# Kernel optimization log

Measured on AMD Instinct MI355X. Metric: run time of the kernel, lower is better.

## Reference

```python
import jax, jax.numpy as jnp
import numpy as np

N_EMBD = 1024
N_HEAD = 16
HEAD_SIZE = N_EMBD // N_HEAD
EPS = 1e-5


def layernorm(x, g, b):
    mu = jnp.mean(x, axis=-1, keepdims=True)
    var = jnp.var(x, axis=-1, keepdims=True)
    return (x - mu) * jax.lax.rsqrt(var + EPS) * g + b


def setup_inputs() -> dict:
    key = jax.random.key(0)
    ks = jax.random.split(key, 12)
    s = 0.02
    C = N_EMBD
    return {
        "x": jax.random.normal(ks[0], (2, 2048, C), dtype=jnp.float32),
        "Wq": jax.random.normal(ks[1], (C, C), dtype=jnp.float32) * s,
        "Wk": jax.random.normal(ks[2], (C, C), dtype=jnp.float32) * s,
        "Wv": jax.random.normal(ks[3], (C, C), dtype=jnp.float32) * s,
        "Wo": jax.random.normal(ks[4], (C, C), dtype=jnp.float32) * s,
        "bo": jnp.zeros((C,), dtype=jnp.float32),
        "W1": jax.random.normal(ks[5], (C, 4 * C), dtype=jnp.float32) * s,
        "b1": jnp.zeros((4 * C,), dtype=jnp.float32),
        "W2": jax.random.normal(ks[6], (4 * C, C), dtype=jnp.float32) * s,
        "b2": jnp.zeros((C,), dtype=jnp.float32),
        "ln1_g": jnp.ones((C,), dtype=jnp.float32),
        "ln1_b": jnp.zeros((C,), dtype=jnp.float32),
        "ln2_g": jnp.ones((C,), dtype=jnp.float32),
        "ln2_b": jnp.zeros((C,), dtype=jnp.float32),
    }


def reference(x, Wq, Wk, Wv, Wo, bo, W1, b1, W2, b2, ln1_g, ln1_b, ln2_g, ln2_b):
    B, T, C = x.shape
    H, Dh = N_HEAD, HEAD_SIZE

    # --- self-attention branch ---
    h = layernorm(x, ln1_g, ln1_b)
    q = (h @ Wq).reshape(B, T, H, Dh)
    k = (h @ Wk).reshape(B, T, H, Dh)
    v = (h @ Wv).reshape(B, T, H, Dh)

    # NOTE: original scales by C**-0.5 (n_embd), not head_size**-0.5
    scale = C ** (-0.5)
    scores = jnp.einsum("bqhd,bkhd->bhqk", q, k) * scale  # [B,H,T,T]
    causal = jnp.tril(jnp.ones((T, T), dtype=bool))
    scores = jnp.where(causal, scores, -jnp.inf)
    wei = jax.nn.softmax(scores, axis=-1)
    attn = jnp.einsum("bhqk,bkhd->bqhd", wei, v).reshape(B, T, C)
    x = x + attn @ Wo + bo

    # --- MLP branch ---
    h2 = layernorm(x, ln2_g, ln2_b)
    ff = jax.nn.relu(h2 @ W1 + b1) @ W2 + b2
    return x + ff
```

## Files before the change

kernel.cpp:

```cpp
#include <hip/hip_runtime.h>

typedef unsigned short u16;
typedef __bf16 bf16;
typedef bf16 bf16x8 __attribute__((ext_vector_type(8)));
typedef float f32x4 __attribute__((ext_vector_type(4)));


__device__ __forceinline__ u16 f2bf(float f) {
  bf16 b = (bf16)f;
  return __builtin_bit_cast(u16, b);
}

__device__ __forceinline__ void gll16(void* lds, const void* g) {
  __builtin_amdgcn_global_load_lds((__attribute__((address_space(1))) void*)g,
                                   (__attribute__((address_space(3))) void*)lds,
                                   16, 0, 0);
}

__device__ __forceinline__ f32x4 mfma16(bf16x8 a, bf16x8 b, f32x4 c) {
  return __builtin_amdgcn_mfma_f32_16x16x32_bf16(a, b, c, 0, 0, 0);
}


__global__ __launch_bounds__(256)
void transpose_all(const float* __restrict__ Wq, const float* __restrict__ Wk,
                   const float* __restrict__ Wv, const float* __restrict__ Wo,
                   const float* __restrict__ W1, const float* __restrict__ W2,
                   u16* __restrict__ WqT, u16* __restrict__ WkT,
                   u16* __restrict__ WvT, u16* __restrict__ WoT,
                   u16* __restrict__ W1T, u16* __restrict__ W2T) {
  __shared__ float tile[32][33];
  const int id = blockIdx.x;
  const float* src;
  u16* dst;
  int R, C, t;
  if (id < 4096) {
    const int w = id >> 10;
    t = id & 1023; R = 1024; C = 1024;
    src = w == 0 ? Wq : w == 1 ? Wk : w == 2 ? Wv : Wo;
    dst = w == 0 ? WqT : w == 1 ? WkT : w == 2 ? WvT : WoT;
  } else if (id < 8192) {
    t = id - 4096; R = 1024; C = 4096; src = W1; dst = W1T;
  } else {
    t = id - 8192; R = 4096; C = 1024; src = W2; dst = W2T;
  }
  const int tilesx = C >> 5;
  const int c0 = (t % tilesx) * 32, r0 = (t / tilesx) * 32;
  const int tx = threadIdx.x, ty = threadIdx.y;
#pragma unroll
  for (int i = 0; i < 4; ++i)
    tile[ty + i * 8][tx] = src[(size_t)(r0 + ty + i * 8) * C + c0 + tx];
  __syncthreads();
#pragma unroll
  for (int i = 0; i < 4; ++i)
    dst[(size_t)(c0 + ty + i * 8) * R + r0 + tx] = f2bf(tile[tx][ty + i * 8]);
}


__global__ __launch_bounds__(256)
void ln_kernel(const float* __restrict__ x, const float* __restrict__ g,
               const float* __restrict__ bb, u16* __restrict__ h) {
  const int row = blockIdx.x;
  const int tid = threadIdx.x;
  const float4 xv = ((const float4*)(x + (size_t)row * 1024))[tid];
  float s = xv.x + xv.y + xv.z + xv.w;
  float q = xv.x * xv.x + xv.y * xv.y + xv.z * xv.z + xv.w * xv.w;
#pragma unroll
  for (int m = 1; m < 64; m <<= 1) {
    s += __shfl_xor(s, m);
    q += __shfl_xor(q, m);
  }
  __shared__ float ss[4], qq[4];
  const int wid = tid >> 6, lane = tid & 63;
  if (lane == 0) { ss[wid] = s; qq[wid] = q; }
  __syncthreads();
  s = ss[0] + ss[1] + ss[2] + ss[3];
  q = qq[0] + qq[1] + qq[2] + qq[3];
  const float mean = s * (1.0f / 1024.0f);
  const float var = q * (1.0f / 1024.0f) - mean * mean;
  const float rs = rsqrtf(var + 1e-5f);
  const float4 gv = ((const float4*)g)[tid];
  const float4 bv = ((const float4*)bb)[tid];
  ushort4 o;
  o.x = f2bf((xv.x - mean) * rs * gv.x + bv.x);
  o.y = f2bf((xv.y - mean) * rs * gv.y + bv.y);
  o.z = f2bf((xv.z - mean) * rs * gv.z + bv.z);
  o.w = f2bf((xv.w - mean) * rs * gv.w + bv.w);
  ((ushort4*)(h + (size_t)row * 1024))[tid] = o;
}


__device__ __forceinline__ void xcd_swizzle(int& bx, int& by, int& bz) {
  const int gx = gridDim.x, gy = gridDim.y;
  const int nwg = gx * gy * (int)gridDim.z;
  int flat = (int)blockIdx.x + gx * ((int)blockIdx.y + gy * (int)blockIdx.z);
  flat = (flat & 7) * (nwg >> 3) + (flat >> 3);
  bx = flat % gx;
  const int rem = flat / gx;
  by = rem % gy;
  bz = rem / gy;
}


template <int EPI>
__global__ __launch_bounds__(256)
void gemm_bt(const u16* __restrict__ A, const u16* __restrict__ Bt,
             const float* __restrict__ bias,
             void* __restrict__ O0, void* __restrict__ O1, void* __restrict__ O2,
             int M, int N, int K) {
  __shared__ __align__(16) u16 Alds[3][128 * 32];
  __shared__ __align__(16) u16 Blds[3][128 * 32];
  const int tid = threadIdx.x;
  const int lane = tid & 63, wid = tid >> 6;
  const int rl = lane & 15, kg = lane >> 4;
  const int ksw = (rl >> 1) & 3;
  int bx, by, bz;
  xcd_swizzle(bx, by, bz);
  const int m0 = by * 128, n0 = bx * 128;
  f32x4 acc[4][4];
#pragma unroll
  for (int i = 0; i < 4; ++i)
#pragma unroll
    for (int j = 0; j < 4; ++j) acc[i][j] = (f32x4){0.f, 0.f, 0.f, 0.f};
  const int wr = wid >> 1, wc = wid & 1;
  const int c0 = wid * 2, c1 = wid * 2 + 1;
  const int srow0 = c0 * 16 + (lane >> 2);
  const int srow1 = c1 * 16 + (lane >> 2);
  const int skol = (((lane & 3) ^ ((lane >> 3) & 3))) * 8;

#define STAGE_BT(buf, k0)                                                      \
  {                                                                            \
    gll16(Alds[buf] + c0 * 512, A + (size_t)(m0 + srow0) * K + (k0) + skol);   \
    gll16(Alds[buf] + c1 * 512, A + (size_t)(m0 + srow1) * K + (k0) + skol);   \
    gll16(Blds[buf] + c0 * 512, Bt + (size_t)(n0 + srow0) * K + (k0) + skol);  \
    gll16(Blds[buf] + c1 * 512, Bt + (size_t)(n0 + srow1) * K + (k0) + skol);  \
  }

  const int nt = K >> 5;
  STAGE_BT(0, 0);
  STAGE_BT(1, 32);
  int cur = 0;
  for (int t = 0; t < nt; ++t) {
    if (t + 1 < nt)
      asm volatile("s_waitcnt vmcnt(4)" ::: "memory");
    else
      asm volatile("s_waitcnt vmcnt(0)" ::: "memory");
    __builtin_amdgcn_s_barrier();
    if (t + 2 < nt) {
      const int nxt = cur >= 1 ? cur - 1 : cur + 2;
      STAGE_BT(nxt, (t + 2) << 5);
    }
    bf16x8 af[4], bfr[4];
#pragma unroll
    for (int m = 0; m < 4; ++m)
      af[m] = *(const bf16x8*)(Alds[cur] + (wr * 64 + m * 16 + rl) * 32 +
                               (kg ^ ksw) * 8);
#pragma unroll
    for (int n = 0; n < 4; ++n)
      bfr[n] = *(const bf16x8*)(Blds[cur] + (wc * 64 + n * 16 + rl) * 32 +
                                (kg ^ ksw) * 8);
    __builtin_amdgcn_s_setprio(1);
#pragma unroll
    for (int m = 0; m < 4; ++m)
#pragma unroll
      for (int n = 0; n < 4; ++n)
        acc[m][n] = mfma16(af[m], bfr[n], acc[m][n]);
    __builtin_amdgcn_s_setprio(0);
    cur = cur + 1 == 3 ? 0 : cur + 1;
  }
#undef STAGE_BT

#pragma unroll
  for (int m = 0; m < 4; ++m) {
#pragma unroll
    for (int n = 0; n < 4; ++n) {
      const int col = n0 + wc * 64 + n * 16 + rl;
      const int row0 = m0 + wr * 64 + m * 16 + kg * 4;
      if (EPI == 0) {
        const int seg = col >> 10;
        const int lc = col & 1023;
        if (seg == 2) {
          u16* vt = (u16*)O2;
          const size_t off =
              ((size_t)((row0 >> 11) * 16 + (lc >> 6)) * 64 + (lc & 63)) * 2048 +
              (row0 & 2047);
          ushort4 pk = {f2bf(acc[m][n][0]), f2bf(acc[m][n][1]),
                        f2bf(acc[m][n][2]), f2bf(acc[m][n][3])};
          *(ushort4*)(vt + off) = pk;
        } else {
          u16* o = (u16*)(seg == 0 ? O0 : O1);
#pragma unroll
          for (int r = 0; r < 4; ++r)
            o[(size_t)(row0 + r) * 1024 + lc] = f2bf(acc[m][n][r]);
        }
      } else {
        const float bv = bias[col];
#pragma unroll
        for (int r = 0; r < 4; ++r) {
          float v = acc[m][n][r] + bv;
          v = v > 0.f ? v : 0.f;
          ((u16*)O0)[(size_t)(row0 + r) * N + col] = f2bf(v);
        }
      }
    }
  }
}


__global__ __launch_bounds__(256)
void gemm64(const u16* __restrict__ A, const u16* __restrict__ Bt,
            const float* __restrict__ bias, const float* __restrict__ res,
            float* __restrict__ O, int M, int N, int K) {
  __shared__ __align__(16) u16 Alds[3][64 * 64];
  __shared__ __align__(16) u16 Blds[3][128 * 64];
  const int tid = threadIdx.x;
  const int lane = tid & 63, wid = tid >> 6;
  const int rl = lane & 15, kg = lane >> 4;
  int bx, by, bz;
  xcd_swizzle(bx, by, bz);
  const int m0 = by * 64, n0 = bx * 128;
  f32x4 acc[2][4];
#pragma unroll
  for (int i = 0; i < 2; ++i)
#pragma unroll
    for (int j = 0; j < 4; ++j) acc[i][j] = (f32x4){0.f, 0.f, 0.f, 0.f};
  const int wr = wid >> 1, wc = wid & 1;
  const int lrow = lane >> 3;
  const int lslot = lane & 7;

#define SRCA(base_r, k0)                                                       \
  (A + (size_t)(m0 + (base_r) + lrow) * K + (k0) +                             \
   ((lslot ^ (((base_r) + lrow) & 7)) * 8))
#define SRCB(base_r, k0)                                                       \
  (Bt + (size_t)(n0 + (base_r) + lrow) * K + (k0) +                            \
   ((lslot ^ (((base_r) + lrow) & 7)) * 8))

#define STAGE_64(buf, k0)                                                      \
  {                                                                            \
    gll16(Alds[buf] + (wid * 16 + 0) * 64, SRCA(wid * 16 + 0, k0));            \
    gll16(Alds[buf] + (wid * 16 + 8) * 64, SRCA(wid * 16 + 8, k0));            \
    gll16(Blds[buf] + (wid * 32 + 0) * 64, SRCB(wid * 32 + 0, k0));            \
    gll16(Blds[buf] + (wid * 32 + 8) * 64, SRCB(wid * 32 + 8, k0));            \
    gll16(Blds[buf] + (wid * 32 + 16) * 64, SRCB(wid * 32 + 16, k0));          \
    gll16(Blds[buf] + (wid * 32 + 24) * 64, SRCB(wid * 32 + 24, k0));          \
  }

  const int nt = K >> 6;
  STAGE_64(0, 0);
  STAGE_64(1, 64);
  int cur = 0;
  for (int t = 0; t < nt; ++t) {
    if (t + 1 < nt)
      asm volatile("s_waitcnt vmcnt(6)" ::: "memory");
    else
      asm volatile("s_waitcnt vmcnt(0)" ::: "memory");
    __builtin_amdgcn_s_barrier();
    if (t + 2 < nt) {
      const int nxt = cur >= 1 ? cur - 1 : cur + 2;
      STAGE_64(nxt, (t + 2) << 6);
    }
    bf16x8 af[2][2], bfr[4][2];
#pragma unroll
    for (int m = 0; m < 2; ++m) {
      const int row = wr * 32 + m * 16 + rl;
#pragma unroll
      for (int kf = 0; kf < 2; ++kf)
        af[m][kf] = *(const bf16x8*)(Alds[cur] + row * 64 +
                                     ((kf * 4 + kg) ^ (row & 7)) * 8);
    }
#pragma unroll
    for (int n = 0; n < 4; ++n) {
      const int row = wc * 64 + n * 16 + rl;
#pragma unroll
      for (int kf = 0; kf < 2; ++kf)
        bfr[n][kf] = *(const bf16x8*)(Blds[cur] + row * 64 +
                                      ((kf * 4 + kg) ^ (row & 7)) * 8);
    }
    __builtin_amdgcn_s_setprio(1);
#pragma unroll
    for (int m = 0; m < 2; ++m)
#pragma unroll
      for (int n = 0; n < 4; ++n) {
        acc[m][n] = mfma16(af[m][0], bfr[n][0], acc[m][n]);
        acc[m][n] = mfma16(af[m][1], bfr[n][1], acc[m][n]);
      }
    __builtin_amdgcn_s_setprio(0);
    cur = cur + 1 == 3 ? 0 : cur + 1;
  }
#undef STAGE_64
#undef SRCA
#undef SRCB

#pragma unroll
  for (int m = 0; m < 2; ++m) {
#pragma unroll
    for (int n = 0; n < 4; ++n) {
      const int col = n0 + wc * 64 + n * 16 + rl;
      const int row0 = m0 + wr * 32 + m * 16 + kg * 4;
      const float bv = bias[col];
#pragma unroll
      for (int r = 0; r < 4; ++r) {
        const int row = row0 + r;
        O[(size_t)row * N + col] =
            acc[m][n][r] + bv + res[(size_t)row * N + col];
      }
    }
  }
}


#define SC2 0.045084220027780106f

__device__ __forceinline__ void attn_range(
    const u16* __restrict__ qg, const u16* __restrict__ kgl,
    const u16* __restrict__ vtb, size_t rowb, int cb, char* plw,
    int rl, int kg, int q0, int kvb, int kve, bool mask_last,
    f32x4 (&ot)[2][4], float (&lrun)[2]) {
  if (kvb >= kve) return;
  const int swz = (rl & 7) << 4;
  bf16x8 qf[2][2];
#pragma unroll
  for (int m = 0; m < 2; ++m) {
    const u16* qp = qg + (rowb + q0 + m * 16 + rl) * 1024 + cb + kg * 8;
    qf[m][0] = *(const bf16x8*)(qp);
    qf[m][1] = *(const bf16x8*)(qp + 32);
  }

  bf16x8 ka[4][2], kb[4][2];
#define LOADK(dst, kvi)                                                        \
  {                                                                            \
    const u16* krow = kgl + (rowb + (kvi) * 64 + rl) * 1024 + cb + kg * 8;     \
    _Pragma("unroll") for (int n = 0; n < 4; ++n) {                            \
      dst[n][0] = *(const bf16x8*)(krow + (size_t)n * 16 * 1024);              \
      dst[n][1] = *(const bf16x8*)(krow + (size_t)n * 16 * 1024 + 32);         \
    }                                                                          \
  }

#define BODY(kf, kvi)                                                          \
  {                                                                            \
    const int kv0 = (kvi) * 64;                                                \
    const u16* vrow = vtb + (size_t)rl * 2048 + kv0 + kg * 8;                  \
    bf16x8 vfr[4][2];                                                          \
    _Pragma("unroll") for (int dt = 0; dt < 4; ++dt) {                         \
      vfr[dt][0] = *(const bf16x8*)(vrow + (size_t)dt * 16 * 2048);            \
      vfr[dt][1] = *(const bf16x8*)(vrow + (size_t)dt * 16 * 2048 + 32);       \
    }                                                                          \
    const bool domask = mask_last && ((kvi) == kve - 1);                       \
    _Pragma("unroll") for (int m = 0; m < 2; ++m) {                            \
      f32x4 s[4];                                                              \
      __builtin_amdgcn_s_setprio(1);                                           \
      _Pragma("unroll") for (int n = 0; n < 4; ++n) {                          \
        f32x4 t = (f32x4){0.f, 0.f, 0.f, 0.f};                                 \
        t = mfma16(kf[n][0], qf[m][0], t);                                     \
        t = mfma16(kf[n][1], qf[m][1], t);                                     \
        s[n] = t;                                                              \
      }                                                                        \
      __builtin_amdgcn_s_setprio(0);                                           \
      if (domask) {                                                            \
        const int qrow = q0 + m * 16 + rl;                                     \
        _Pragma("unroll") for (int n = 0; n < 4; ++n)                          \
            _Pragma("unroll") for (int r = 0; r < 4; ++r) {                    \
          const int tk = kv0 + n * 16 + 4 * kg + r;                            \
          s[n][r] = (tk > qrow) ? -3e38f : s[n][r];                            \
        }                                                                      \
      }                                                                        \
      float ps = 0.f;                                                          \
      _Pragma("unroll") for (int n = 0; n < 4; ++n) {                          \
        const float p0 = exp2f(__builtin_fmaf(s[n][0], SC2, -8.f));            \
        const float p1 = exp2f(__builtin_fmaf(s[n][1], SC2, -8.f));            \
        const float p2 = exp2f(__builtin_fmaf(s[n][2], SC2, -8.f));            \
        const float p3 = exp2f(__builtin_fmaf(s[n][3], SC2, -8.f));            \
        ps += (p0 + p1) + (p2 + p3);                                           \
        ushort4 pk = {f2bf(p0), f2bf(p1), f2bf(p2), f2bf(p3)};                 \
        *(ushort4*)(plw + m * 2048 + ((rl * 128 + n * 32 + kg * 8) ^ swz)) =   \
            pk;                                                                \
      }                                                                        \
      lrun[m] += ps;                                                           \
    }                                                                          \
    _Pragma("unroll") for (int m = 0; m < 2; ++m) {                            \
      const bf16x8 pf0 =                                                       \
          *(const bf16x8*)(plw + m * 2048 + ((rl * 128 + kg * 16) ^ swz));     \
      const bf16x8 pf1 = *(const bf16x8*)(plw + m * 2048 +                     \
                                          ((rl * 128 + 64 + kg * 16) ^ swz));  \
      __builtin_amdgcn_s_setprio(1);                                           \
      _Pragma("unroll") for (int dt = 0; dt < 4; ++dt) {                       \
        ot[m][dt] = mfma16(vfr[dt][0], pf0, ot[m][dt]);                        \
        ot[m][dt] = mfma16(vfr[dt][1], pf1, ot[m][dt]);                        \
      }                                                                        \
      __builtin_amdgcn_s_setprio(0);                                           \
    }                                                                          \
  }

  LOADK(ka, kvb);
  int kv = kvb;
  for (;;) {
    if (kv + 1 < kve) LOADK(kb, kv + 1);
    BODY(ka, kv);
    ++kv;
    if (kv >= kve) break;
    if (kv + 1 < kve) LOADK(ka, kv + 1);
    BODY(kb, kv);
    ++kv;
    if (kv >= kve) break;
  }
#undef LOADK
#undef BODY
}

__global__ __launch_bounds__(128)
void attn_kernel(const u16* __restrict__ qg, const u16* __restrict__ kgl,
                 const u16* __restrict__ vtg, u16* __restrict__ og) {
  const int tid = threadIdx.x, lane = tid & 63, wid = tid >> 6;
  const int rl = lane & 15, kg = lane >> 4;
  const int flat = blockIdx.x;
  const int bh = (flat & 7) * 4 + ((flat >> 3) & 3);
  const int pr = flat >> 5;
  const int jA = pr, jB = 63 - pr;
  const int nA = (jA >> 1) + 1, nB = (jB >> 1) + 1;
  const int a = (nB - nA) >> 1;
  const size_t rowb = (size_t)(bh >> 4) * 2048;
  const int cb = (bh & 15) * 64;
  const u16* vtb = vtg + (size_t)bh * 64 * 2048;

  __shared__ __align__(16) char Pl[2][4096];
  __shared__ __align__(16) float MrgO[2][4][64][4];
  __shared__ float MrgL[2][16];
  char* plw = Pl[wid];

  f32x4 ot[2][4];
  float lrun[2] = {0.f, 0.f};
#pragma unroll
  for (int m = 0; m < 2; ++m)
#pragma unroll
    for (int dt = 0; dt < 4; ++dt) ot[m][dt] = (f32x4){0.f, 0.f, 0.f, 0.f};

  if (wid == 0) {
    attn_range(qg, kgl, vtb, rowb, cb, plw, rl, kg, jA * 32, 0, nA, true,
               ot, lrun);
#pragma unroll
    for (int m = 0; m < 2; ++m) {
      lrun[m] += __shfl_xor(lrun[m], 16);
      lrun[m] += __shfl_xor(lrun[m], 32);
      const float inv = 1.f / lrun[m];
      u16* orow = og + (rowb + jA * 32 + m * 16 + rl) * 1024 + cb;
#pragma unroll
      for (int dt = 0; dt < 4; ++dt) {
        ushort4 ok = {f2bf(ot[m][dt][0] * inv), f2bf(ot[m][dt][1] * inv),
                      f2bf(ot[m][dt][2] * inv), f2bf(ot[m][dt][3] * inv)};
        *(ushort4*)(orow + dt * 16 + 4 * kg) = ok;
      }
      lrun[m] = 0.f;
#pragma unroll
      for (int dt = 0; dt < 4; ++dt) ot[m][dt] = (f32x4){0.f, 0.f, 0.f, 0.f};
    }
    attn_range(qg, kgl, vtb, rowb, cb, plw, rl, kg, jB * 32, 0, a, false,
               ot, lrun);
  } else {
    attn_range(qg, kgl, vtb, rowb, cb, plw, rl, kg, jB * 32, a, nB, true,
               ot, lrun);
#pragma unroll
    for (int m = 0; m < 2; ++m) {
      lrun[m] += __shfl_xor(lrun[m], 16);
      lrun[m] += __shfl_xor(lrun[m], 32);
#pragma unroll
      for (int dt = 0; dt < 4; ++dt)
        *(f32x4*)(&MrgO[m][dt][lane][0]) = ot[m][dt];
      if (kg == 0) MrgL[m][rl] = lrun[m];
    }
  }
  __syncthreads();
  if (wid == 0) {
#pragma unroll
    for (int m = 0; m < 2; ++m) {
      lrun[m] += __shfl_xor(lrun[m], 16);
      lrun[m] += __shfl_xor(lrun[m], 32);
      const float inv = 1.f / (lrun[m] + MrgL[m][rl]);
      u16* orow = og + (rowb + jB * 32 + m * 16 + rl) * 1024 + cb;
#pragma unroll
      for (int dt = 0; dt < 4; ++dt) {
        const f32x4 o1 = *(const f32x4*)(&MrgO[m][dt][lane][0]);
        ushort4 ok;
#pragma unroll
        for (int r = 0; r < 4; ++r)
          ((u16*)&ok)[r] = f2bf((ot[m][dt][r] + o1[r]) * inv);
        *(ushort4*)(orow + dt * 16 + 4 * kg) = ok;
      }
    }
  }
}


extern "C" void kernel_launch(void* const* d_in, const int* in_sizes, int n_in,
                              void* d_out, int out_size, void* d_ws, size_t ws_size,
                              hipStream_t stream) {
  const float* x    = (const float*)d_in[0];
  const float* Wq   = (const float*)d_in[1];
  const float* Wk   = (const float*)d_in[2];
  const float* Wv   = (const float*)d_in[3];
  const float* Wo   = (const float*)d_in[4];
  const float* bo   = (const float*)d_in[5];
  const float* W1   = (const float*)d_in[6];
  const float* b1   = (const float*)d_in[7];
  const float* W2   = (const float*)d_in[8];
  const float* b2   = (const float*)d_in[9];
  const float* ln1g = (const float*)d_in[10];
  const float* ln1b = (const float*)d_in[11];
  const float* ln2g = (const float*)d_in[12];
  const float* ln2b = (const float*)d_in[13];
  float* out = (float*)d_out;

  char* ws = (char*)d_ws;
  const size_t MB = 1024 * 1024;
  u16* WqT  = (u16*)(ws + 0 * MB);
  u16* WoT  = (u16*)(ws + 6 * MB);
  u16* W1T  = (u16*)(ws + 8 * MB);
  u16* W2T  = (u16*)(ws + 16 * MB);
  u16* h    = (u16*)(ws + 24 * MB);
  u16* q    = (u16*)(ws + 32 * MB);
  u16* k    = (u16*)(ws + 40 * MB);
  u16* vt   = (u16*)(ws + 48 * MB);
  u16* attn = (u16*)(ws + 56 * MB);
  float* x1 = (float*)(ws + 64 * MB);
  u16* ff1  = (u16*)(ws + 32 * MB);
  u16* WkT  = WqT + 1024 * 1024;
  u16* WvT  = WqT + 2 * 1024 * 1024;

  dim3 tblk(32, 8);
  transpose_all<<<12288, tblk, 0, stream>>>(Wq, Wk, Wv, Wo, W1, W2,
                                            WqT, WkT, WvT, WoT, W1T, W2T);

  ln_kernel<<<4096, 256, 0, stream>>>(x, ln1g, ln1b, h);

  gemm_bt<0><<<dim3(24, 32), 256, 0, stream>>>(h, WqT, nullptr,
                                               q, k, vt, 4096, 3072, 1024);

  attn_kernel<<<1024, 128, 0, stream>>>(q, k, vt, attn);

  gemm64<<<dim3(8, 64), 256, 0, stream>>>(attn, WoT, bo, x, x1,
                                          4096, 1024, 1024);

  ln_kernel<<<4096, 256, 0, stream>>>(x1, ln2g, ln2b, h);

  gemm_bt<1><<<dim3(32, 32), 256, 0, stream>>>(h, W1T, b1, ff1, ff1, ff1,
                                               4096, 4096, 1024);

  gemm64<<<dim3(8, 64), 256, 0, stream>>>(ff1, W2T, b2, x1, out,
                                          4096, 1024, 4096);
}
```

Baseline: 254.9 us.

## Use 64-wide K tiles with double buffering and 8-slot XOR swizzle in GEMM

The GEMM K-step grows from 32 to 64 and the LDS pipeline drops from triple to double buffering, with a second barrier after compute before the freed buffer is refilled. LDS rows become 64 elements wide with an 8-slot XOR swizzle, and each iteration issues two MFMAs per output tile. This halves the number of barriers and loop iterations per K and amortizes the waitcnts, but it adds a barrier per step and shortens the prefetch distance. That may expose more global-load latency.

```diff
diff --git a/kernel.cpp b/kernel.cpp
--- a/kernel.cpp
+++ b/kernel.cpp
@@ -108,12 +108,11 @@
              const float* __restrict__ bias,
              void* __restrict__ O0, void* __restrict__ O1, void* __restrict__ O2,
              int M, int N, int K) {
-  __shared__ __align__(16) u16 Alds[3][128 * 32];
-  __shared__ __align__(16) u16 Blds[3][128 * 32];
+  __shared__ __align__(16) u16 Alds[2][128 * 64];
+  __shared__ __align__(16) u16 Blds[2][128 * 64];
   const int tid = threadIdx.x;
   const int lane = tid & 63, wid = tid >> 6;
   const int rl = lane & 15, kg = lane >> 4;
-  const int ksw = (rl >> 1) & 3;
   int bx, by, bz;
   xcd_swizzle(bx, by, bz);
   const int m0 = by * 128, n0 = bx * 128;
@@ -123,52 +122,70 @@
 #pragma unroll
     for (int j = 0; j < 4; ++j) acc[i][j] = (f32x4){0.f, 0.f, 0.f, 0.f};
   const int wr = wid >> 1, wc = wid & 1;
-  const int c0 = wid * 2, c1 = wid * 2 + 1;
-  const int srow0 = c0 * 16 + (lane >> 2);
-  const int srow1 = c1 * 16 + (lane >> 2);
-  const int skol = (((lane & 3) ^ ((lane >> 3) & 3))) * 8;
+  const int lrow = lane >> 3;
+  const int lslot = lane & 7;
+
+#define SRCA(base_r, k0)                                                       \
+  (A + (size_t)(m0 + (base_r) + lrow) * K + (k0) +                             \
+   ((lslot ^ (((base_r) + lrow) & 7)) * 8))
+#define SRCB(base_r, k0)                                                       \
+  (Bt + (size_t)(n0 + (base_r) + lrow) * K + (k0) +                            \
+   ((lslot ^ (((base_r) + lrow) & 7)) * 8))
 
 #define STAGE_BT(buf, k0)                                                      \
   {                                                                            \
-    gll16(Alds[buf] + c0 * 512, A + (size_t)(m0 + srow0) * K + (k0) + skol);   \
-    gll16(Alds[buf] + c1 * 512, A + (size_t)(m0 + srow1) * K + (k0) + skol);   \
-    gll16(Blds[buf] + c0 * 512, Bt + (size_t)(n0 + srow0) * K + (k0) + skol);  \
-    gll16(Blds[buf] + c1 * 512, Bt + (size_t)(n0 + srow1) * K + (k0) + skol);  \
-  }
-
-  const int nt = K >> 5;
+    gll16(Alds[buf] + (wid * 32 + 0) * 64, SRCA(wid * 32 + 0, k0));            \
+    gll16(Alds[buf] + (wid * 32 + 8) * 64, SRCA(wid * 32 + 8, k0));            \
+    gll16(Alds[buf] + (wid * 32 + 16) * 64, SRCA(wid * 32 + 16, k0));          \
+    gll16(Alds[buf] + (wid * 32 + 24) * 64, SRCA(wid * 32 + 24, k0));          \
+    gll16(Blds[buf] + (wid * 32 + 0) * 64, SRCB(wid * 32 + 0, k0));            \
+    gll16(Blds[buf] + (wid * 32 + 8) * 64, SRCB(wid * 32 + 8, k0));            \
+    gll16(Blds[buf] + (wid * 32 + 16) * 64, SRCB(wid * 32 + 16, k0));          \
+    gll16(Blds[buf] + (wid * 32 + 24) * 64, SRCB(wid * 32 + 24, k0));          \
+  }
+
+  const int nt = K >> 6;
   STAGE_BT(0, 0);
-  STAGE_BT(1, 32);
-  int cur = 0;
+  STAGE_BT(1, 64);
   for (int t = 0; t < nt; ++t) {
+    const int cur = t & 1;
     if (t + 1 < nt)
-      asm volatile("s_waitcnt vmcnt(4)" ::: "memory");
+      asm volatile("s_waitcnt vmcnt(8)" ::: "memory");
     else
       asm volatile("s_waitcnt vmcnt(0)" ::: "memory");
     __builtin_amdgcn_s_barrier();
-    if (t + 2 < nt) {
-      const int nxt = cur >= 1 ? cur - 1 : cur + 2;
-      STAGE_BT(nxt, (t + 2) << 5);
-    }
-    bf16x8 af[4], bfr[4];
+    bf16x8 af[4][2], bfr[4][2];
+#pragma unroll
+    for (int m = 0; m < 4; ++m) {
+      const int row = wr * 64 + m * 16 + rl;
+#pragma unroll
+      for (int kf = 0; kf < 2; ++kf)
+        af[m][kf] = *(const bf16x8*)(Alds[cur] + row * 64 +
+                                     ((kf * 4 + kg) ^ (row & 7)) * 8);
+    }
+#pragma unroll
+    for (int n = 0; n < 4; ++n) {
+      const int row = wc * 64 + n * 16 + rl;
+#pragma unroll
+      for (int kf = 0; kf < 2; ++kf)
+        bfr[n][kf] = *(const bf16x8*)(Blds[cur] + row * 64 +
+                                      ((kf * 4 + kg) ^ (row & 7)) * 8);
+    }
+    __builtin_amdgcn_s_setprio(1);
 #pragma unroll
     for (int m = 0; m < 4; ++m)
-      af[m] = *(const bf16x8*)(Alds[cur] + (wr * 64 + m * 16 + rl) * 32 +
-                               (kg ^ ksw) * 8);
-#pragma unroll
-    for (int n = 0; n < 4; ++n)
-      bfr[n] = *(const bf16x8*)(Blds[cur] + (wc * 64 + n * 16 + rl) * 32 +
-                                (kg ^ ksw) * 8);
-    __builtin_amdgcn_s_setprio(1);
-#pragma unroll
-    for (int m = 0; m < 4; ++m)
-#pragma unroll
-      for (int n = 0; n < 4; ++n)
-        acc[m][n] = mfma16(af[m], bfr[n], acc[m][n]);
+#pragma unroll
+      for (int n = 0; n < 4; ++n) {
+        acc[m][n] = mfma16(af[m][0], bfr[n][0], acc[m][n]);
+        acc[m][n] = mfma16(af[m][1], bfr[n][1], acc[m][n]);
+      }
     __builtin_amdgcn_s_setprio(0);
-    cur = cur + 1 == 3 ? 0 : cur + 1;
+    __builtin_amdgcn_s_barrier();
+    if (t + 2 < nt) STAGE_BT(cur, (t + 2) << 6);
   }
 #undef STAGE_BT
+#undef SRCA
+#undef SRCB
 
 #pragma unroll
   for (int m = 0; m < 4; ++m) {
```

Result: no change. 257.7 us (+1.1%).
